# Performance work log

Hardware: AMD Instinct MI355X
Metric: run time of the kernel (lower is better)

## Reference

```python
import jax, jax.numpy as jnp
import numpy as np

NUM_REL = 3


def _edge_norm(dst, et, n_nodes):
    # PyG RGCNConv default aggr='mean': mean over edges per (dst, relation).
    seg = dst * NUM_REL + et
    cnt = jax.ops.segment_sum(jnp.ones(dst.shape[0], jnp.float32), seg,
                              num_segments=n_nodes * NUM_REL)
    return 1.0 / jnp.maximum(cnt, 1.0)[seg], seg  # [E]


def _rgcn_layer(x, W, root, b, src, dst, et, norm_e, seg, transform_first):
    n = x.shape[0]
    if transform_first:
        # h_r = x @ W_r for all relations, gather message per edge, scatter-add.
        H = jnp.einsum('ni,rio->rno', x, W)          # [R, N, out]
        m = H[et, src] * norm_e[:, None]             # [E, out]
        agg = jax.ops.segment_sum(m, dst, num_segments=n)
    else:
        # mean-aggregate in input space first (mean commutes with linear map).
        m = x[src] * norm_e[:, None]                 # [E, in]
        A = jax.ops.segment_sum(m, seg, num_segments=n * NUM_REL)
        A = A.reshape(n, NUM_REL, -1)                # [N, R, in]
        agg = jnp.einsum('nri,rio->no', A, W)
    return agg + x @ root + b


def _make_params(key, in_c, out_c):
    dims = [(in_c, 1024), (1024, 512), (512, 128)]
    ks = jax.random.split(key, 14)
    p = {}
    for li, (i, o) in enumerate(dims, start=1):
        p[f'W{li}'] = jax.random.normal(ks[3 * li - 3], (NUM_REL, i, o), jnp.float32) * 0.02
        p[f'root{li}'] = jax.random.normal(ks[3 * li - 2], (i, o), jnp.float32) * 0.02
        p[f'b{li}'] = jnp.zeros((o,), jnp.float32)
    p['fc_w'] = jax.random.normal(ks[9], (128, out_c), jnp.float32) * 0.02
    p['fc_b'] = jnp.zeros((out_c,), jnp.float32)
    return p


def setup_inputs() -> dict:
    key = jax.random.key(0)
    N, E, IN_C, OUT_C = 40000, 500000, 256, 21
    k1, k2, k3, k4 = jax.random.split(key, 4)
    inp = {
        'x': jax.random.normal(k1, (N, IN_C), jnp.float32),
        'edge_index': jax.random.randint(k2, (2, E), 0, N, jnp.int64)
            if jax.config.jax_enable_x64 else jax.random.randint(k2, (2, E), 0, N, jnp.int32),
        'edge_type': jax.random.randint(k3, (E,), 0, NUM_REL, jnp.int32),
    }
    inp.update(_make_params(k4, IN_C, OUT_C))
    return inp


def reference(x, edge_index, edge_type, W1, root1, b1, W2, root2, b2,
              W3, root3, b3, fc_w, fc_b):
    src, dst = edge_index[0], edge_index[1]
    et = edge_type
    n = x.shape[0]
    norm_e, seg = _edge_norm(dst, et, n)
    # layer 1: in(256) < out(1024) -> aggregate-first is cheaper
    h = _rgcn_layer(x, W1, root1, b1, src, dst, et, norm_e, seg, transform_first=False)
    h = jax.nn.relu(h)  # dropout is identity in eval mode
    # layer 2: in(1024) > out(512) -> transform-first
    h = _rgcn_layer(h, W2, root2, b2, src, dst, et, norm_e, seg, transform_first=True)
    h = jax.nn.relu(h)
    # layer 3: in(512) > out(128) -> transform-first
    h = _rgcn_layer(h, W3, root3, b3, src, dst, et, norm_e, seg, transform_first=True)
    h = jax.nn.relu(h)
    logits = h @ fc_w + fc_b
    return jax.nn.log_softmax(logits, axis=1)
```

## Files before the change

kernel.cpp:

```cpp
#include <hip/hip_runtime.h>
#include <cstdint>
#include <cstddef>


typedef short bf16x8 __attribute__((ext_vector_type(8)));
typedef float f32x4 __attribute__((ext_vector_type(4)));

#define GF_BIAS 1
#define GF_RELU 2
#define GF_BF16 4

__device__ __forceinline__ unsigned short f2bf(float f) {
    unsigned u = __float_as_uint(f);
    return (unsigned short)((u + 0x7FFFu + ((u >> 16) & 1u)) >> 16);
}
__device__ __forceinline__ float bf2f(unsigned short h) {
    return __uint_as_float((unsigned)h << 16);
}

__global__ __launch_bounds__(256) void zero_kernel(float* __restrict__ p, long n4)
{
    long i = (long)blockIdx.x * 256 + threadIdx.x;
    if (i < n4) ((float4*)p)[i] = make_float4(0.f, 0.f, 0.f, 0.f);
}

__global__ __launch_bounds__(256) void count_kernel(
    const int* __restrict__ dst, const int* __restrict__ et,
    int* __restrict__ cnt, int E)
{
    int e = blockIdx.x * 256 + threadIdx.x;
    if (e < E) atomicAdd(&cnt[dst[e] * 3 + et[e]], 1);
}

__global__ __launch_bounds__(256) void scanA(
    const int* __restrict__ cnt, int* __restrict__ base,
    int* __restrict__ bsum, int S)
{
    __shared__ int sh[256];
    int i = blockIdx.x * 256 + threadIdx.x;
    int v = (i < S) ? cnt[i] : 0;
    sh[threadIdx.x] = v;
    __syncthreads();
#pragma unroll
    for (int off = 1; off < 256; off <<= 1) {
        int t = (threadIdx.x >= off) ? sh[threadIdx.x - off] : 0;
        __syncthreads();
        sh[threadIdx.x] += t;
        __syncthreads();
    }
    if (i < S) base[i] = sh[threadIdx.x] - v;
    if (threadIdx.x == 255) bsum[blockIdx.x] = sh[255];
}

__global__ __launch_bounds__(512) void scanB(int* __restrict__ bsum, int NB)
{
    __shared__ int sh[512];
    int t = threadIdx.x;
    int v = (t < NB) ? bsum[t] : 0;
    sh[t] = v;
    __syncthreads();
#pragma unroll
    for (int off = 1; off < 512; off <<= 1) {
        int u = (t >= off) ? sh[t - off] : 0;
        __syncthreads();
        sh[t] += u;
        __syncthreads();
    }
    if (t < NB) bsum[t] = sh[t] - v;
}

__global__ __launch_bounds__(256) void scanC(
    int* __restrict__ base, const int* __restrict__ bsum, int S)
{
    int i = blockIdx.x * 256 + threadIdx.x;
    if (i < S) base[i] += bsum[blockIdx.x];
}

__global__ __launch_bounds__(256) void fill_kernel(
    const int* __restrict__ src, const int* __restrict__ dst,
    const int* __restrict__ et, int* __restrict__ base,
    int* __restrict__ cnt, int* __restrict__ elist, int E, int S)
{
    int e = blockIdx.x * 256 + threadIdx.x;
    if (e == 0) base[S] = E;
    if (e >= E) return;
    int seg = dst[e] * 3 + et[e];
    int old = atomicSub(&cnt[seg], 1);
    elist[base[seg] + old - 1] = src[e];
}

__global__ __launch_bounds__(256) void tr1_tiled(
    const float* __restrict__ W1, const float* __restrict__ root1,
    unsigned short* __restrict__ W1t)
{
    __shared__ float sh[32][33];
    int bk = blockIdx.x & 31, bj = blockIdx.x >> 5;
    int tc = threadIdx.x & 31, tr = threadIdx.x >> 5;
    int k0 = bk * 32, j0 = bj * 32;
#pragma unroll
    for (int i = 0; i < 4; ++i) {
        int k = k0 + tr + i * 8;
        float v = (k < 768) ? W1[(size_t)k * 1024 + j0 + tc]
                            : root1[(size_t)(k - 768) * 1024 + j0 + tc];
        sh[tr + i * 8][tc] = v;
    }
    __syncthreads();
#pragma unroll
    for (int i = 0; i < 4; ++i)
        W1t[(size_t)(j0 + tr + i * 8) * 1024 + k0 + tc] = f2bf(sh[tc][tr + i * 8]);
}

__global__ __launch_bounds__(256) void tr2_tiled(
    const float* __restrict__ root2, const float* __restrict__ W2,
    unsigned short* __restrict__ W2cat)
{
    __shared__ float sh[32][33];
    int bk = blockIdx.x & 31, br = blockIdx.x >> 5;
    int tc = threadIdx.x & 31, tr = threadIdx.x >> 5;
    int k0 = bk * 32, r0 = br * 32;
    int s = r0 >> 9, j0 = r0 & 511;
    const float* src = (s == 0) ? root2 : W2 + (size_t)(s - 1) * 524288;
#pragma unroll
    for (int i = 0; i < 4; ++i)
        sh[tr + i * 8][tc] = src[(size_t)(k0 + tr + i * 8) * 512 + j0 + tc];
    __syncthreads();
#pragma unroll
    for (int i = 0; i < 4; ++i)
        W2cat[(size_t)(r0 + tr + i * 8) * 1024 + k0 + tc] = f2bf(sh[tc][tr + i * 8]);
}

__global__ __launch_bounds__(256) void tr3_tiled(
    const float* __restrict__ root3, const float* __restrict__ W3,
    unsigned short* __restrict__ W3cat)
{
    __shared__ float sh[32][33];
    int bk = blockIdx.x & 15, br = blockIdx.x >> 4;
    int tc = threadIdx.x & 31, tr = threadIdx.x >> 5;
    int k0 = bk * 32, r0 = br * 32;
    int s = r0 >> 7, j0 = r0 & 127;
    const float* src = (s == 0) ? root3 : W3 + (size_t)(s - 1) * 65536;
#pragma unroll
    for (int i = 0; i < 4; ++i)
        sh[tr + i * 8][tc] = src[(size_t)(k0 + tr + i * 8) * 128 + j0 + tc];
    __syncthreads();
#pragma unroll
    for (int i = 0; i < 4; ++i)
        W3cat[(size_t)(r0 + tr + i * 8) * 512 + k0 + tc] = f2bf(sh[tc][tr + i * 8]);
}

__global__ __launch_bounds__(256) void bias_cat(
    float* __restrict__ b2cat, float* __restrict__ b3cat,
    const float* __restrict__ b2, const float* __restrict__ b3)
{
    int i = blockIdx.x * 256 + threadIdx.x;
    if (i < 2048) b2cat[i] = (i < 512) ? b2[i] : 0.f;
    else if (i < 2560) { int j = i - 2048; b3cat[j] = (j < 128) ? b3[j] : 0.f; }
}

__global__ __launch_bounds__(256) void conv_bf16(
    const float* __restrict__ s, unsigned short* __restrict__ d, long n8)
{
    long i = (long)blockIdx.x * 256 + threadIdx.x;
    if (i >= n8) return;
    const float* p = s + i * 8;
    float4 a = *(const float4*)p, b = *(const float4*)(p + 4);
    ushort4 o0, o1;
    o0.x = f2bf(a.x); o0.y = f2bf(a.y); o0.z = f2bf(a.z); o0.w = f2bf(a.w);
    o1.x = f2bf(b.x); o1.y = f2bf(b.y); o1.z = f2bf(b.z); o1.w = f2bf(b.w);
    *(ushort4*)(d + i * 8) = o0;
    *(ushort4*)(d + i * 8 + 4) = o1;
}

__global__ __launch_bounds__(256) void agg1_kernel(
    const unsigned short* __restrict__ xb, const int* __restrict__ base,
    const int* __restrict__ elist, unsigned short* __restrict__ Xcat)
{
    int n = blockIdx.x;
    int w = threadIdx.x >> 6, l = threadIdx.x & 63;
    if (w == 3) {
        *(ushort4*)&Xcat[(size_t)n * 1024 + 768 + l * 4] =
            *(const ushort4*)&xb[(size_t)n * 256 + l * 4];
        return;
    }
    int seg = n * 3 + w;
    int st = base[seg], len = base[seg + 1] - st;
    float norm = 1.0f / (float)(len > 0 ? len : 1);
    float4 s = make_float4(0.f, 0.f, 0.f, 0.f);
    for (int i = 0; i < len; ++i) {
        int sx = elist[st + i];
        ushort4 v = *(const ushort4*)&xb[(size_t)sx * 256 + l * 4];
        s.x += bf2f(v.x); s.y += bf2f(v.y); s.z += bf2f(v.z); s.w += bf2f(v.w);
    }
    ushort4 o;
    o.x = f2bf(s.x * norm); o.y = f2bf(s.y * norm);
    o.z = f2bf(s.z * norm); o.w = f2bf(s.w * norm);
    *(ushort4*)&Xcat[(size_t)n * 1024 + w * 256 + l * 4] = o;
}

__global__ __launch_bounds__(128) void agg2_fused(
    const unsigned short* __restrict__ H2all, unsigned short* __restrict__ h2b,
    const int* __restrict__ base, const int* __restrict__ elist)
{
    int n = blockIdx.x, t = threadIdx.x;
    ushort4 rv = *(const ushort4*)&H2all[(size_t)n * 2048 + t * 4];
    float4 a = make_float4(bf2f(rv.x), bf2f(rv.y), bf2f(rv.z), bf2f(rv.w));
#pragma unroll
    for (int r = 0; r < 3; ++r) {
        int seg = n * 3 + r;
        int st = base[seg], len = base[seg + 1] - st;
        float norm = 1.0f / (float)(len > 0 ? len : 1);
        float4 s = make_float4(0.f, 0.f, 0.f, 0.f);
        for (int i = 0; i < len; ++i) {
            int sx = elist[st + i];
            ushort4 v = *(const ushort4*)&H2all[(size_t)sx * 2048 + 512 * (1 + r) + t * 4];
            s.x += bf2f(v.x); s.y += bf2f(v.y); s.z += bf2f(v.z); s.w += bf2f(v.w);
        }
        a.x += s.x * norm; a.y += s.y * norm; a.z += s.z * norm; a.w += s.w * norm;
    }
    ushort4 o;
    o.x = f2bf(fmaxf(a.x, 0.f)); o.y = f2bf(fmaxf(a.y, 0.f));
    o.z = f2bf(fmaxf(a.z, 0.f)); o.w = f2bf(fmaxf(a.w, 0.f));
    *(ushort4*)&h2b[(size_t)n * 512 + t * 4] = o;
}

__global__ __launch_bounds__(128) void agg2_inc(
    const unsigned short* __restrict__ H2q, float* __restrict__ h2acc,
    unsigned short* __restrict__ h2b, const int* __restrict__ base,
    const int* __restrict__ elist, int r, int last)
{
    int n = blockIdx.x, t = threadIdx.x;
    int seg = n * 3 + r;
    int st = base[seg], len = base[seg + 1] - st;
    float norm = 1.0f / (float)(len > 0 ? len : 1);
    float4 s = make_float4(0.f, 0.f, 0.f, 0.f);
    for (int i = 0; i < len; ++i) {
        int sx = elist[st + i];
        ushort4 v = *(const ushort4*)&H2q[(size_t)sx * 512 + t * 4];
        s.x += bf2f(v.x); s.y += bf2f(v.y); s.z += bf2f(v.z); s.w += bf2f(v.w);
    }
    float4 a = *(const float4*)&h2acc[(size_t)n * 512 + t * 4];
    a.x += s.x * norm; a.y += s.y * norm; a.z += s.z * norm; a.w += s.w * norm;
    if (!last) {
        *(float4*)&h2acc[(size_t)n * 512 + t * 4] = a;
    } else {
        ushort4 o;
        o.x = f2bf(fmaxf(a.x, 0.f)); o.y = f2bf(fmaxf(a.y, 0.f));
        o.z = f2bf(fmaxf(a.z, 0.f)); o.w = f2bf(fmaxf(a.w, 0.f));
        *(ushort4*)&h2b[(size_t)n * 512 + t * 4] = o;
    }
}

__global__ __launch_bounds__(256) void agg3_head(
    const unsigned short* __restrict__ H3cat, const float* __restrict__ fcw,
    const float* __restrict__ fcb, const int* __restrict__ base,
    const int* __restrict__ elist, float* __restrict__ out)
{
    __shared__ float sh[4][128];
    int wid = threadIdx.x >> 6, lane = threadIdx.x & 63;
    int n = blockIdx.x * 4 + wid;
    ushort2 rt = *(const ushort2*)&H3cat[(size_t)n * 512 + lane * 2];
    float s0 = bf2f(rt.x), s1 = bf2f(rt.y);
#pragma unroll
    for (int r = 0; r < 3; ++r) {
        int seg = n * 3 + r;
        int st = base[seg], len = base[seg + 1] - st;
        float norm = 1.0f / (float)(len > 0 ? len : 1);
        float t0 = 0.f, t1 = 0.f;
        for (int i = 0; i < len; ++i) {
            int sx = elist[st + i];
            ushort2 v = *(const ushort2*)&H3cat[(size_t)sx * 512 + 128 * (1 + r) + lane * 2];
            t0 += bf2f(v.x); t1 += bf2f(v.y);
        }
        s0 += t0 * norm; s1 += t1 * norm;
    }
    sh[wid][lane * 2]     = fmaxf(s0, 0.f);
    sh[wid][lane * 2 + 1] = fmaxf(s1, 0.f);
    __syncthreads();
    float logit = 0.f;
    if (lane < 21) {
        logit = fcb[lane];
#pragma unroll
        for (int k = 0; k < 128; ++k) logit += sh[wid][k] * fcw[k * 21 + lane];
    }
    float v = (lane < 21) ? logit : -INFINITY;
#pragma unroll
    for (int off = 32; off; off >>= 1) v = fmaxf(v, __shfl_xor(v, off));
    float mx = v;
    float ex = (lane < 21) ? expf(logit - mx) : 0.f;
#pragma unroll
    for (int off = 32; off; off >>= 1) ex += __shfl_xor(ex, off);
    if (lane < 21) out[(size_t)n * 21 + lane] = logit - mx - logf(ex);
}

__global__ __launch_bounds__(256) void gemm_mfma(
    const unsigned short* __restrict__ A, const unsigned short* __restrict__ Bt,
    const float* __restrict__ bias, void* __restrict__ C,
    int Nout, int K, int flags, int lgGX)
{
    __shared__ short __align__(16) As[8192];
    __shared__ short __align__(16) Bs[8192];
    const int tid = threadIdx.x;
    const int w = tid >> 6, l = tid & 63;

    const int nblk = (int)gridDim.x;
    const int q = nblk >> 3, rem = nblk & 7;
    const int xcd = blockIdx.x & 7, local = blockIdx.x >> 3;
    const int id2 = xcd * q + (xcd < rem ? xcd : rem) + local;
    const int row0 = (id2 >> lgGX) * 128;
    const int col0 = (id2 & ((1 << lgGX) - 1)) * 128;

    const int wm = w >> 1, wn = w & 1;
    const int lr = l >> 3, lc = l & 7;

    f32x4 acc[4][4];
#pragma unroll
    for (int i = 0; i < 4; ++i)
#pragma unroll
        for (int j = 0; j < 4; ++j) acc[i][j] = (f32x4){0.f, 0.f, 0.f, 0.f};

    for (int k0 = 0; k0 < K; k0 += 64) {
        __syncthreads();
#pragma unroll
        for (int i = 0; i < 4; ++i) {
            const int c  = i * 4 + w;
            const int r  = c * 8 + lr;
            const int c8 = lc ^ (r & 7);
            __builtin_amdgcn_global_load_lds(
                (const __attribute__((address_space(1))) void*)
                    (A + (size_t)(row0 + r) * K + k0 + c8 * 8),
                (__attribute__((address_space(3))) void*)(As + c * 512),
                16, 0, 0);
            __builtin_amdgcn_global_load_lds(
                (const __attribute__((address_space(1))) void*)
                    (Bt + (size_t)(col0 + r) * K + k0 + c8 * 8),
                (__attribute__((address_space(3))) void*)(Bs + c * 512),
                16, 0, 0);
        }
        __syncthreads();
#pragma unroll
        for (int ks = 0; ks < 2; ++ks) {
            bf16x8 af[4], bfv[4];
#pragma unroll
            for (int mf = 0; mf < 4; ++mf) {
                int r = wm * 64 + mf * 16 + (l & 15);
                int byt = (r * 128 + ks * 64 + (l >> 4) * 16) ^ ((r & 7) << 4);
                af[mf] = *(const bf16x8*)((const char*)As + byt);
            }
#pragma unroll
            for (int nf = 0; nf < 4; ++nf) {
                int r = wn * 64 + nf * 16 + (l & 15);
                int byt = (r * 128 + ks * 64 + (l >> 4) * 16) ^ ((r & 7) << 4);
                bfv[nf] = *(const bf16x8*)((const char*)Bs + byt);
            }
#pragma unroll
            for (int mf = 0; mf < 4; ++mf)
#pragma unroll
                for (int nf = 0; nf < 4; ++nf)
                    acc[mf][nf] = __builtin_amdgcn_mfma_f32_16x16x32_bf16(
                        af[mf], bfv[nf], acc[mf][nf], 0, 0, 0);
        }
    }

    const int lrow = (l >> 4) * 4;
    const int lcol = l & 15;
#pragma unroll
    for (int mf = 0; mf < 4; ++mf) {
#pragma unroll
        for (int nf = 0; nf < 4; ++nf) {
            int col = col0 + wn * 64 + nf * 16 + lcol;
            float bv = (flags & GF_BIAS) ? bias[col] : 0.f;
#pragma unroll
            for (int rr = 0; rr < 4; ++rr) {
                int row = row0 + wm * 64 + mf * 16 + lrow + rr;
                float v = acc[mf][nf][rr] + bv;
                if (flags & GF_RELU) v = fmaxf(v, 0.f);
                size_t idx = (size_t)row * Nout + col;
                if (flags & GF_BF16) ((unsigned short*)C)[idx] = f2bf(v);
                else                 ((float*)C)[idx] = v;
            }
        }
    }
}

extern "C" void kernel_launch(void* const* d_in, const int* in_sizes, int n_in,
                              void* d_out, int out_size, void* d_ws, size_t ws_size,
                              hipStream_t stream)
{
    const float* x     = (const float*)d_in[0];
    const int*   ei    = (const int*)d_in[1];
    const int*   etp   = (const int*)d_in[2];
    const float* W1    = (const float*)d_in[3];
    const float* root1 = (const float*)d_in[4];
    const float* b1    = (const float*)d_in[5];
    const float* W2    = (const float*)d_in[6];
    const float* root2 = (const float*)d_in[7];
    const float* b2    = (const float*)d_in[8];
    const float* W3    = (const float*)d_in[9];
    const float* root3 = (const float*)d_in[10];
    const float* b3    = (const float*)d_in[11];
    const float* fcw   = (const float*)d_in[12];
    const float* fcb   = (const float*)d_in[13];
    float* out = (float*)d_out;
    (void)n_in; (void)out_size;

    const int N   = in_sizes[0] / 256;
    const int E   = in_sizes[2];
    const int S   = N * 3;
    const int NP  = (N + 127) / 128 * 128;
    const int GY  = NP / 128;
    const int NB  = (S + 255) / 256;
    const int* srcp = ei;
    const int* dstp = ei + E;

    const size_t SZ_X1024 = (size_t)NP * 1024 * 2;
    const size_t SZ_X512b = (size_t)NP * 512 * 2;
    const size_t SZ_X2048 = (size_t)NP * 2048 * 2;

    char* ws = (char*)d_ws;
    int*            cnt   = (int*)(ws + 0);
    int*            base  = (int*)(ws + 480256);
    int*            elist = (int*)(ws + 960512);
    float*          b2cat = (float*)(ws + 2960512);
    float*          b3cat = (float*)(ws + 2968704);
    unsigned short* W3cat = (unsigned short*)(ws + 2970752);
    unsigned short* W2cat = (unsigned short*)(ws + 3495040);
    const size_t fixed_end = 7689344;
    const size_t FUSED_NEED = 7692288 + SZ_X2048 + SZ_X1024;
    const bool fused = ws_size >= FUSED_NEED;

    char* arena;
    unsigned short *W1t, *xb, *Xcat, *h1b, *H2all, *H2q, *h2b, *H3cat;
    float* h2acc;
    if (fused) {
        arena = ws + 7692288;
        Xcat  = (unsigned short*)(arena);
        W1t   = (unsigned short*)(arena + SZ_X1024);
        xb    = (unsigned short*)(arena + SZ_X1024 + 2097152);
        h1b   = (unsigned short*)(arena + SZ_X2048);
        H2all = (unsigned short*)(arena);
        h2b   = (unsigned short*)(arena + SZ_X2048);
        H3cat = (unsigned short*)(arena);
        H2q = nullptr; h2acc = nullptr;
    } else {
        W1t   = (unsigned short*)(ws + fixed_end);
        arena = ws + 9789440;
        Xcat  = (unsigned short*)(arena);
        h2acc = (float*)(arena);
        h1b   = (unsigned short*)(arena + SZ_X1024);
        h2b   = (unsigned short*)(arena + SZ_X1024);
        H3cat = (unsigned short*)(arena + SZ_X1024 + SZ_X512b);
        xb    = (unsigned short*)(arena + 2 * SZ_X1024);
        H2q   = (unsigned short*)(arena + 2 * SZ_X1024);
        H2all = nullptr;
    }
    int* bsum = (int*)(arena);

    zero_kernel<<<(30016 + 255) / 256, 256, 0, stream>>>((float*)cnt, 30016);
    count_kernel<<<(E + 255) / 256, 256, 0, stream>>>(dstp, etp, cnt, E);
    scanA<<<NB, 256, 0, stream>>>(cnt, base, bsum, S);
    scanB<<<1, 512, 0, stream>>>(bsum, NB);
    scanC<<<NB, 256, 0, stream>>>(base, bsum, S);
    fill_kernel<<<(E + 255) / 256, 256, 0, stream>>>(srcp, dstp, etp, base, cnt, elist, E, S);

    tr1_tiled<<<1024, 256, 0, stream>>>(W1, root1, W1t);
    tr2_tiled<<<2048, 256, 0, stream>>>(root2, W2, W2cat);
    tr3_tiled<<<256, 256, 0, stream>>>(root3, W3, W3cat);
    bias_cat<<<10, 256, 0, stream>>>(b2cat, b3cat, b2, b3);
    conv_bf16<<<(int)(((long)N * 32 + 255) / 256), 256, 0, stream>>>(x, xb, (long)N * 32);

    agg1_kernel<<<N, 256, 0, stream>>>(xb, base, elist, Xcat);
    gemm_mfma<<<8 * GY, 256, 0, stream>>>(
        Xcat, W1t, b1, h1b, 1024, 1024, GF_BIAS | GF_RELU | GF_BF16, 3);

    if (fused) {
        gemm_mfma<<<16 * GY, 256, 0, stream>>>(
            h1b, W2cat, b2cat, H2all, 2048, 1024, GF_BIAS | GF_BF16, 4);
        agg2_fused<<<N, 128, 0, stream>>>(H2all, h2b, base, elist);
    } else {
        gemm_mfma<<<4 * GY, 256, 0, stream>>>(
            h1b, W2cat, b2, h2acc, 512, 1024, GF_BIAS, 2);
        for (int r = 0; r < 3; ++r) {
            gemm_mfma<<<4 * GY, 256, 0, stream>>>(
                h1b, W2cat + (size_t)(1 + r) * 524288, nullptr, H2q, 512, 1024, GF_BF16, 2);
            agg2_inc<<<N, 128, 0, stream>>>(H2q, h2acc, h2b, base, elist, r, r == 2);
        }
    }

    gemm_mfma<<<4 * GY, 256, 0, stream>>>(
        h2b, W3cat, b3cat, H3cat, 512, 512, GF_BIAS | GF_BF16, 2);
    agg3_head<<<N / 4, 256, 0, stream>>>(H3cat, fcw, fcb, base, elist, out);
}
```

Measured before the change: 675.5 us.

## Widen gather loads and split edges across lane groups in aggregation kernels

The three edge-aggregation kernels now have each lane load 8 bf16 values (16 bytes) per edge instead of 2 or 4. In agg1 and agg3, groups of lanes handle different edges in parallel and are combined afterwards with cross-lane shuffles. agg2 maps one wavefront per node, four nodes per block, and unrolls the edge loop by two with separate accumulators. The aim is more memory-level parallelism and fewer, wider gather instructions, at the cost of extra shuffle reductions and idle lanes on the final writes.

```diff
diff --git a/kernel.cpp b/kernel.cpp
--- a/kernel.cpp
+++ b/kernel.cpp
@@ -185,42 +185,149 @@
     int seg = n * 3 + w;
     int st = base[seg], len = base[seg + 1] - st;
     float norm = 1.0f / (float)(len > 0 ? len : 1);
-    float4 s = make_float4(0.f, 0.f, 0.f, 0.f);
-    for (int i = 0; i < len; ++i) {
-        int sx = elist[st + i];
-        ushort4 v = *(const ushort4*)&xb[(size_t)sx * 256 + l * 4];
-        s.x += bf2f(v.x); s.y += bf2f(v.y); s.z += bf2f(v.z); s.w += bf2f(v.w);
-    }
-    ushort4 o;
-    o.x = f2bf(s.x * norm); o.y = f2bf(s.y * norm);
-    o.z = f2bf(s.z * norm); o.w = f2bf(s.w * norm);
-    *(ushort4*)&Xcat[(size_t)n * 1024 + w * 256 + l * 4] = o;
-}
-
-__global__ __launch_bounds__(128) void agg2_fused(
+    int g = l >> 5, c8 = (l & 31) * 8;
+    float a[8];
+#pragma unroll
+    for (int j = 0; j < 8; ++j) a[j] = 0.f;
+    for (int i = g; i < len; i += 2) {
+        const unsigned short* q = xb + (size_t)elist[st + i] * 256 + c8;
+        ushort4 v0 = *(const ushort4*)q;
+        ushort4 v1 = *(const ushort4*)(q + 4);
+        a[0] += bf2f(v0.x); a[1] += bf2f(v0.y); a[2] += bf2f(v0.z); a[3] += bf2f(v0.w);
+        a[4] += bf2f(v1.x); a[5] += bf2f(v1.y); a[6] += bf2f(v1.z); a[7] += bf2f(v1.w);
+    }
+#pragma unroll
+    for (int j = 0; j < 8; ++j) a[j] += __shfl_xor(a[j], 32);
+    if (l < 32) {
+        ushort4 o0, o1;
+        o0.x = f2bf(a[0] * norm); o0.y = f2bf(a[1] * norm);
+        o0.z = f2bf(a[2] * norm); o0.w = f2bf(a[3] * norm);
+        o1.x = f2bf(a[4] * norm); o1.y = f2bf(a[5] * norm);
+        o1.z = f2bf(a[6] * norm); o1.w = f2bf(a[7] * norm);
+        unsigned short* d = Xcat + (size_t)n * 1024 + w * 256 + c8;
+        *(ushort4*)d = o0;
+        *(ushort4*)(d + 4) = o1;
+    }
+}
+
+__global__ __launch_bounds__(256) void agg2_fused(
     const unsigned short* __restrict__ H2all, unsigned short* __restrict__ h2b,
     const int* __restrict__ base, const int* __restrict__ elist)
 {
-    int n = blockIdx.x, t = threadIdx.x;
-    ushort4 rv = *(const ushort4*)&H2all[(size_t)n * 2048 + t * 4];
-    float4 a = make_float4(bf2f(rv.x), bf2f(rv.y), bf2f(rv.z), bf2f(rv.w));
+    int w = threadIdx.x >> 6, l = threadIdx.x & 63;
+    int n = blockIdx.x * 4 + w;
+    int c8 = l * 8;
+    const unsigned short* rowN = H2all + (size_t)n * 2048 + c8;
+    float a[8];
+    {
+        ushort4 r0 = *(const ushort4*)rowN;
+        ushort4 r1 = *(const ushort4*)(rowN + 4);
+        a[0] = bf2f(r0.x); a[1] = bf2f(r0.y); a[2] = bf2f(r0.z); a[3] = bf2f(r0.w);
+        a[4] = bf2f(r1.x); a[5] = bf2f(r1.y); a[6] = bf2f(r1.z); a[7] = bf2f(r1.w);
+    }
 #pragma unroll
     for (int r = 0; r < 3; ++r) {
         int seg = n * 3 + r;
         int st = base[seg], len = base[seg + 1] - st;
         float norm = 1.0f / (float)(len > 0 ? len : 1);
-        float4 s = make_float4(0.f, 0.f, 0.f, 0.f);
-        for (int i = 0; i < len; ++i) {
-            int sx = elist[st + i];
-            ushort4 v = *(const ushort4*)&H2all[(size_t)sx * 2048 + 512 * (1 + r) + t * 4];
-            s.x += bf2f(v.x); s.y += bf2f(v.y); s.z += bf2f(v.z); s.w += bf2f(v.w);
-        }
-        a.x += s.x * norm; a.y += s.y * norm; a.z += s.z * norm; a.w += s.w * norm;
-    }
-    ushort4 o;
-    o.x = f2bf(fmaxf(a.x, 0.f)); o.y = f2bf(fmaxf(a.y, 0.f));
-    o.z = f2bf(fmaxf(a.z, 0.f)); o.w = f2bf(fmaxf(a.w, 0.f));
-    *(ushort4*)&h2b[(size_t)n * 512 + t * 4] = o;
+        float p0[8], p1[8];
+#pragma unroll
+        for (int j = 0; j < 8; ++j) { p0[j] = 0.f; p1[j] = 0.f; }
+        int i = 0;
+        for (; i + 2 <= len; i += 2) {
+            const unsigned short* q0 =
+                H2all + (size_t)elist[st + i] * 2048 + 512 * (1 + r) + c8;
+            const unsigned short* q1 =
+                H2all + (size_t)elist[st + i + 1] * 2048 + 512 * (1 + r) + c8;
+            ushort4 u0 = *(const ushort4*)q0, u1 = *(const ushort4*)(q0 + 4);
+            ushort4 v0 = *(const ushort4*)q1, v1 = *(const ushort4*)(q1 + 4);
+            p0[0] += bf2f(u0.x); p0[1] += bf2f(u0.y); p0[2] += bf2f(u0.z); p0[3] += bf2f(u0.w);
+            p0[4] += bf2f(u1.x); p0[5] += bf2f(u1.y); p0[6] += bf2f(u1.z); p0[7] += bf2f(u1.w);
+            p1[0] += bf2f(v0.x); p1[1] += bf2f(v0.y); p1[2] += bf2f(v0.z); p1[3] += bf2f(v0.w);
+            p1[4] += bf2f(v1.x); p1[5] += bf2f(v1.y); p1[6] += bf2f(v1.z); p1[7] += bf2f(v1.w);
+        }
+        if (i < len) {
+            const unsigned short* q0 =
+                H2all + (size_t)elist[st + i] * 2048 + 512 * (1 + r) + c8;
+            ushort4 u0 = *(const ushort4*)q0, u1 = *(const ushort4*)(q0 + 4);
+            p0[0] += bf2f(u0.x); p0[1] += bf2f(u0.y); p0[2] += bf2f(u0.z); p0[3] += bf2f(u0.w);
+            p0[4] += bf2f(u1.x); p0[5] += bf2f(u1.y); p0[6] += bf2f(u1.z); p0[7] += bf2f(u1.w);
+        }
+#pragma unroll
+        for (int j = 0; j < 8; ++j) a[j] += (p0[j] + p1[j]) * norm;
+    }
+    ushort4 o0, o1;
+    o0.x = f2bf(fmaxf(a[0], 0.f)); o0.y = f2bf(fmaxf(a[1], 0.f));
+    o0.z = f2bf(fmaxf(a[2], 0.f)); o0.w = f2bf(fmaxf(a[3], 0.f));
+    o1.x = f2bf(fmaxf(a[4], 0.f)); o1.y = f2bf(fmaxf(a[5], 0.f));
+    o1.z = f2bf(fmaxf(a[6], 0.f)); o1.w = f2bf(fmaxf(a[7], 0.f));
+    unsigned short* d = h2b + (size_t)n * 512 + c8;
+    *(ushort4*)d = o0;
+    *(ushort4*)(d + 4) = o1;
+}
+
+__global__ __launch_bounds__(256) void agg3_head(
+    const unsigned short* __restrict__ H3cat, const float* __restrict__ fcw,
+    const float* __restrict__ fcb, const int* __restrict__ base,
+    const int* __restrict__ elist, float* __restrict__ out)
+{
+    __shared__ float sh[4][128];
+    int wid = threadIdx.x >> 6, lane = threadIdx.x & 63;
+    int n = blockIdx.x * 4 + wid;
+    int g = lane >> 4, c8 = (lane & 15) * 8;
+    float a[8];
+#pragma unroll
+    for (int j = 0; j < 8; ++j) a[j] = 0.f;
+#pragma unroll
+    for (int r = 0; r < 3; ++r) {
+        int seg = n * 3 + r;
+        int st = base[seg], len = base[seg + 1] - st;
+        float norm = 1.0f / (float)(len > 0 ? len : 1);
+        float p[8];
+#pragma unroll
+        for (int j = 0; j < 8; ++j) p[j] = 0.f;
+        for (int i = g; i < len; i += 4) {
+            const unsigned short* q =
+                H3cat + (size_t)elist[st + i] * 512 + 128 * (1 + r) + c8;
+            ushort4 u0 = *(const ushort4*)q, u1 = *(const ushort4*)(q + 4);
+            p[0] += bf2f(u0.x); p[1] += bf2f(u0.y); p[2] += bf2f(u0.z); p[3] += bf2f(u0.w);
+            p[4] += bf2f(u1.x); p[5] += bf2f(u1.y); p[6] += bf2f(u1.z); p[7] += bf2f(u1.w);
+        }
+#pragma unroll
+        for (int j = 0; j < 8; ++j) a[j] += p[j] * norm;
+    }
+#pragma unroll
+    for (int j = 0; j < 8; ++j) {
+        a[j] += __shfl_xor(a[j], 16);
+        a[j] += __shfl_xor(a[j], 32);
+    }
+    if (lane < 16) {
+        const unsigned short* rt = H3cat + (size_t)n * 512 + c8;
+        ushort4 r0 = *(const ushort4*)rt, r1 = *(const ushort4*)(rt + 4);
+        sh[wid][c8 + 0] = fmaxf(a[0] + bf2f(r0.x), 0.f);
+        sh[wid][c8 + 1] = fmaxf(a[1] + bf2f(r0.y), 0.f);
+        sh[wid][c8 + 2] = fmaxf(a[2] + bf2f(r0.z), 0.f);
+        sh[wid][c8 + 3] = fmaxf(a[3] + bf2f(r0.w), 0.f);
+        sh[wid][c8 + 4] = fmaxf(a[4] + bf2f(r1.x), 0.f);
+        sh[wid][c8 + 5] = fmaxf(a[5] + bf2f(r1.y), 0.f);
+        sh[wid][c8 + 6] = fmaxf(a[6] + bf2f(r1.z), 0.f);
+        sh[wid][c8 + 7] = fmaxf(a[7] + bf2f(r1.w), 0.f);
+    }
+    __syncthreads();
+    float logit = 0.f;
+    if (lane < 21) {
+        logit = fcb[lane];
+#pragma unroll
+        for (int k = 0; k < 128; ++k) logit += sh[wid][k] * fcw[k * 21 + lane];
+    }
+    float v = (lane < 21) ? logit : -INFINITY;
+#pragma unroll
+    for (int off = 32; off; off >>= 1) v = fmaxf(v, __shfl_xor(v, off));
+    float mx = v;
+    float ex = (lane < 21) ? expf(logit - mx) : 0.f;
+#pragma unroll
+    for (int off = 32; off; off >>= 1) ex += __shfl_xor(ex, off);
+    if (lane < 21) out[(size_t)n * 21 + lane] = logit - mx - logf(ex);
 }
 
 __global__ __launch_bounds__(128) void agg2_inc(
@@ -248,48 +355,6 @@
         o.z = f2bf(fmaxf(a.z, 0.f)); o.w = f2bf(fmaxf(a.w, 0.f));
         *(ushort4*)&h2b[(size_t)n * 512 + t * 4] = o;
     }
-}
-
-__global__ __launch_bounds__(256) void agg3_head(
-    const unsigned short* __restrict__ H3cat, const float* __restrict__ fcw,
-    const float* __restrict__ fcb, const int* __restrict__ base,
-    const int* __restrict__ elist, float* __restrict__ out)
-{
-    __shared__ float sh[4][128];
-    int wid = threadIdx.x >> 6, lane = threadIdx.x & 63;
-    int n = blockIdx.x * 4 + wid;
-    ushort2 rt = *(const ushort2*)&H3cat[(size_t)n * 512 + lane * 2];
-    float s0 = bf2f(rt.x), s1 = bf2f(rt.y);
-#pragma unroll
-    for (int r = 0; r < 3; ++r) {
-        int seg = n * 3 + r;
-        int st = base[seg], len = base[seg + 1] - st;
-        float norm = 1.0f / (float)(len > 0 ? len : 1);
-        float t0 = 0.f, t1 = 0.f;
-        for (int i = 0; i < len; ++i) {
-            int sx = elist[st + i];
-            ushort2 v = *(const ushort2*)&H3cat[(size_t)sx * 512 + 128 * (1 + r) + lane * 2];
-            t0 += bf2f(v.x); t1 += bf2f(v.y);
-        }
-        s0 += t0 * norm; s1 += t1 * norm;
-    }
-    sh[wid][lane * 2]     = fmaxf(s0, 0.f);
-    sh[wid][lane * 2 + 1] = fmaxf(s1, 0.f);
-    __syncthreads();
-    float logit = 0.f;
-    if (lane < 21) {
-        logit = fcb[lane];
-#pragma unroll
-        for (int k = 0; k < 128; ++k) logit += sh[wid][k] * fcw[k * 21 + lane];
-    }
-    float v = (lane < 21) ? logit : -INFINITY;
-#pragma unroll
-    for (int off = 32; off; off >>= 1) v = fmaxf(v, __shfl_xor(v, off));
-    float mx = v;
-    float ex = (lane < 21) ? expf(logit - mx) : 0.f;
-#pragma unroll
-    for (int off = 32; off; off >>= 1) ex += __shfl_xor(ex, off);
-    if (lane < 21) out[(size_t)n * 21 + lane] = logit - mx - logf(ex);
 }
 
 __global__ __launch_bounds__(256) void gemm_mfma(
@@ -475,7 +540,7 @@
     if (fused) {
         gemm_mfma<<<16 * GY, 256, 0, stream>>>(
             h1b, W2cat, b2cat, H2all, 2048, 1024, GF_BIAS | GF_BF16, 4);
-        agg2_fused<<<N, 128, 0, stream>>>(H2all, h2b, base, elist);
+        agg2_fused<<<N / 4, 256, 0, stream>>>(H2all, h2b, base, elist);
     } else {
         gemm_mfma<<<4 * GY, 256, 0, stream>>>(
             h1b, W2cat, b2, h2acc, 512, 1024, GF_BIAS, 2);
```

After: 626.4 us. -7.3%, faster.
